# Kernel optimization log

Measured on AMD Instinct MI355X. Metric: run time of the kernel, lower is better.

Reference implementation:

```python
import jax, jax.numpy as jnp
import numpy as np

B, N, D, H = 8, 2048, 128, 8
HD = D // H  # head_depth = 16
CLIP = 10.0
INF = 1e10
THETA = 10000.0
SCALE_BASE = 512.0
LOGIT_SCALE = float(np.log(400.0) / np.log(50.0) / np.sqrt(HD))


def _rotate_half(x):
    # interleaved pairs: (x1, x2) -> (-x2, x1)
    x1 = x[..., ::2]
    x2 = x[..., 1::2]
    return jnp.stack((-x2, x1), axis=-1).reshape(x.shape)


def _rope_xpos(n, hd):
    # rotary_embedding_torch RotaryEmbedding(dim=hd, use_xpos=True)
    inv_freq = 1.0 / (THETA ** (jnp.arange(0, hd, 2, dtype=jnp.float32) / hd))  # (hd/2,)
    t = jnp.arange(n, dtype=jnp.float32)
    freqs = t[:, None] * inv_freq[None, :]          # (n, hd/2)
    freqs = jnp.repeat(freqs, 2, axis=-1)           # (n, hd) interleaved dup
    sc = (jnp.arange(0, hd, 2, dtype=jnp.float32) + 0.4 * hd) / (1.4 * hd)  # (hd/2,)
    power = (t - (n // 2)) / SCALE_BASE             # centered positions
    scale = sc[None, :] ** power[:, None]           # (n, hd/2)
    scale = jnp.repeat(scale, 2, axis=-1)           # (n, hd)
    return freqs, scale


def setup_inputs() -> dict:
    key = jax.random.key(0)
    ks = jax.random.split(key, 7)
    stdv_qkv = 1.0 / np.sqrt(HD)
    stdv_out = 1.0 / np.sqrt(D)
    q = jax.random.normal(ks[0], (B, N, D), dtype=jnp.float32)
    k = jax.random.normal(ks[1], (B, N, D), dtype=jnp.float32)
    v = jax.random.normal(ks[2], (B, N, D), dtype=jnp.float32)
    Wq = jax.random.uniform(ks[3], (D, D), minval=-stdv_qkv, maxval=stdv_qkv, dtype=jnp.float32)
    Wk = jax.random.uniform(ks[4], (D, D), minval=-stdv_qkv, maxval=stdv_qkv, dtype=jnp.float32)
    Wv = jax.random.uniform(ks[5], (D, D), minval=-stdv_qkv, maxval=stdv_qkv, dtype=jnp.float32)
    Wout = jax.random.uniform(ks[6], (D, D), minval=-stdv_out, maxval=stdv_out, dtype=jnp.float32)
    mask = jnp.zeros((B, N, 1), dtype=bool)
    return {"q": q, "k": k, "v": v, "Wq": Wq, "Wk": Wk, "Wv": Wv, "Wout": Wout, "mask": mask}


def reference(q, k, v, Wq, Wk, Wv, Wout, mask):
    def split_heads(t, W):
        # torch Linear (bias=False): t @ W.T, then (B,N,H,HD) -> (B,H,N,HD)
        return (t @ W.T).reshape(B, N, H, HD).transpose(0, 2, 1, 3)

    Qh = split_heads(q, Wq)
    Kh = split_heads(k, Wk)
    Vh = split_heads(v, Wv)

    freqs, scale = _rope_xpos(N, HD)  # (N, HD) each, broadcast over (B,H,N,HD)
    cos, sin = jnp.cos(freqs), jnp.sin(freqs)
    Qr = Qh * (cos * scale) + _rotate_half(Qh) * (sin * scale)
    inv_scale = 1.0 / scale
    Kr = Kh * (cos * inv_scale) + _rotate_half(Kh) * (sin * inv_scale)

    logits = jnp.einsum('bhqd,bhkd->bhqk', Qr, Kr) * LOGIT_SCALE
    logits = CLIP * jnp.tanh(logits)
    # mask: (B,N,1) bool, True -> masked; broadcast to (B,1,1,N)
    logits = jnp.where(mask[:, None, None, :, 0], -INF, logits)
    probs = jax.nn.softmax(logits, axis=-1)
    out = jnp.einsum('bhqk,bhkd->bhqd', probs, Vh)
    out = out.transpose(0, 2, 1, 3).reshape(B, N, D)
    return out @ Wout.T
```

## Files before the change

kernel.cpp:

```cpp
#include <hip/hip_runtime.h>
#include <math.h>

#define BB 8
#define NN 2048
#define DD 128
#define HH 8

typedef _Float16 v4h __attribute__((ext_vector_type(4)));
typedef _Float16 v8h __attribute__((ext_vector_type(8)));
typedef float    v4f __attribute__((ext_vector_type(4)));
typedef float    v16f __attribute__((ext_vector_type(16)));

__device__ __forceinline__ v4f zero4() { v4f z = {0.f, 0.f, 0.f, 0.f}; return z; }
__device__ __forceinline__ v16f zero16() {
    v16f z;
    #pragma unroll
    for (int i = 0; i < 16; ++i) z[i] = 0.f;
    return z;
}

__device__ __forceinline__ v4f mfma16(v4h a, v4h b, v4f c) {
    return __builtin_amdgcn_mfma_f32_16x16x16f16(a, b, c, 0, 0, 0);
}
__device__ __forceinline__ v16f mfma32(v8h a, v8h b, v16f c) {
    return __builtin_amdgcn_mfma_f32_32x32x16_f16(a, b, c, 0, 0, 0);
}

__device__ __forceinline__ float fexp2(float x) {
#if __has_builtin(__builtin_amdgcn_exp2f)
    return __builtin_amdgcn_exp2f(x);
#else
    return __expf(x * 0.69314718055994531f);
#endif
}

#define QSCALE 1.10478088f
#define C1F 14.426950408889634f
#define C2F 28.853900817779268f

__global__ __launch_bounds__(256) void prep_kernel(
    const float* __restrict__ Wq, const float* __restrict__ Wk,
    const float* __restrict__ Wv, const float* __restrict__ Wo,
    _Float16* __restrict__ WH, _Float16* __restrict__ WoH,
    float* __restrict__ rtab)
{
    int tid = blockIdx.x * 256 + threadIdx.x;
    int m = tid >> 14, i = tid & 16383;
    const float* src = (m == 0) ? Wq : (m == 1) ? Wk : (m == 2) ? Wv : Wo;
    float wv = src[i];
    if (m < 3) WH[m * 16384 + i] = (_Float16)wv;
    else       WoH[i] = (_Float16)wv;

    if (tid < NN * 16) {
        int t = tid >> 4, hd = tid & 15, j = hd >> 1;
        const float invf_tab[8] = {1.f, 0.31622776601683794f, 0.1f, 0.031622776601683791f,
                                   0.01f, 0.0031622776601683794f, 0.001f, 0.00031622776601683794f};
        float freq = (float)t * invf_tab[j];
        float c = cosf(freq), s = sinf(freq);
        float scf = ((float)(2 * j) + 6.4f) / 22.4f;
        float pw  = ((float)t - 1024.0f) / 512.0f;
        float scl = exp2f(pw * log2f(scf));
        rtab[0 * NN * 16 + tid] = c * scl * QSCALE;
        rtab[1 * NN * 16 + tid] = s * scl * QSCALE;
        float is = 1.0f / scl;
        rtab[2 * NN * 16 + tid] = c * is;
        rtab[3 * NN * 16 + tid] = s * is;
    }
}

__global__ __launch_bounds__(256) void proj_rope_kernel(
    const float* __restrict__ q, const float* __restrict__ k, const float* __restrict__ v,
    const _Float16* __restrict__ WH, const float* __restrict__ rtab,
    _Float16* __restrict__ Qr, _Float16* __restrict__ Kr, _Float16* __restrict__ VT)
{
    __shared__ __align__(16) _Float16 xb[64][136];
    const int tid = threadIdx.x;
    const int m  = blockIdx.y;
    const int r0 = blockIdx.x * 64;
    const int b  = r0 >> 11;
    const int n0 = r0 & 2047;

    const float* s = ((m == 0) ? q : (m == 1) ? k : v) + (size_t)r0 * 128;
    #pragma unroll
    for (int i = 0; i < 8; ++i) {
        int u = tid + i * 256;
        int row = u >> 5, c4 = (u & 31) * 4;
        v4f f = *(const v4f*)(s + row * 128 + c4);
        v4h hv; hv[0]=(_Float16)f[0]; hv[1]=(_Float16)f[1]; hv[2]=(_Float16)f[2]; hv[3]=(_Float16)f[3];
        *(v4h*)&xb[row][c4] = hv;
    }
    __syncthreads();

    const int w = tid >> 6, lane = tid & 63;
    const int l16 = lane & 15, quad = lane >> 4;

    v4h xf[8];
    #pragma unroll
    for (int kt = 0; kt < 8; ++kt)
        xf[kt] = *(const v4h*)&xb[w * 16 + l16][kt * 16 + quad * 4];
    const _Float16* Wm = WH + m * 16384;
    v4f acc[8];
    #pragma unroll
    for (int ct = 0; ct < 8; ++ct) acc[ct] = zero4();
    #pragma unroll
    for (int kt = 0; kt < 8; ++kt) {
        #pragma unroll
        for (int ct = 0; ct < 8; ++ct) {
            v4h wf = *(const v4h*)(Wm + (ct * 16 + l16) * 128 + kt * 16 + quad * 4);
            if (m < 2) acc[ct] = mfma16(wf, xf[kt], acc[ct]);
            else       acc[ct] = mfma16(xf[kt], wf, acc[ct]);
        }
    }
    if (m < 2) {
        const float* tc = rtab + (m == 0 ? 0 : 2 * NN * 16);
        const float* ts = tc + NN * 16;
        const int n = n0 + w * 16 + l16;
        _Float16* dst = (m == 0 ? Qr : Kr);
        #pragma unroll
        for (int ct = 0; ct < 8; ++ct) {
            v4f cs = *(const v4f*)(tc + n * 16 + quad * 4);
            v4f sn = *(const v4f*)(ts + n * 16 + quad * 4);
            v4f a = acc[ct];
            v4f rot; rot[0] = -a[1]; rot[1] = a[0]; rot[2] = -a[3]; rot[3] = a[2];
            v4h o;
            #pragma unroll
            for (int r = 0; r < 4; ++r) o[r] = (_Float16)(a[r] * cs[r] + rot[r] * sn[r]);
            *(v4h*)(dst + ((size_t)(b * 8 + ct) * NN + n) * 16 + quad * 4) = o;
        }
    } else {
        #pragma unroll
        for (int ct = 0; ct < 8; ++ct) {
            v4f a = acc[ct];
            v4h o;
            #pragma unroll
            for (int r = 0; r < 4; ++r) o[r] = (_Float16)a[r];
            *(v4h*)(VT + ((size_t)(b * 8 + ct) * 16 + l16) * NN + n0 + w * 16 + quad * 4) = o;
        }
    }
}

__global__ __launch_bounds__(256, 4) void attn_kernel(
    const _Float16* __restrict__ Qr, const _Float16* __restrict__ Kr,
    const _Float16* __restrict__ VT, const unsigned char* __restrict__ mask,
    _Float16* __restrict__ Obuf)
{
    __shared__ __align__(16) char smem[15360];
    _Float16* Kt = (_Float16*)smem;
    _Float16* Ve = (_Float16*)(smem + 6144);
    float*    av = (float*)(smem + 14848);

    const int tid = threadIdx.x;
    const int bh = blockIdx.x >> 4;
    const int qt = blockIdx.x & 15;
    const int b = bh >> 3, h = bh & 7;
    const int q0 = qt * 128;
    const int w = tid >> 6, lane = tid & 63;
    const int l32 = lane & 31, hi = lane >> 5;

    const int qrow = q0 + w * 32 + l32;
    v8h qf = *(const v8h*)(Qr + ((size_t)bh * NN + qrow) * 16 + hi * 8);

    {
        v8h one8;
        #pragma unroll
        for (int i = 0; i < 8; ++i) one8[i] = (_Float16)1.f;
        *(v8h*)(Ve + (16 + (tid >> 4)) * 136 + (tid & 15) * 8) = one8;
    }

    v16f acc = zero16();

    const int krow = tid >> 1, kpar = tid & 1;
    const int vhd = tid >> 4, vg = tid & 15;
    const _Float16* Kbase = Kr + (size_t)bh * NN * 16;
    const _Float16* Vbase = VT + ((size_t)bh * 16 + vhd) * NN;
    const unsigned char* mbase = mask + b * NN;

    v8h kv = *(const v8h*)(Kbase + (size_t)krow * 16 + kpar * 8);
    v8h vv = *(const v8h*)(Vbase + vg * 8);
    float adv = 0.f;
    if (tid < 128) adv = mbase[tid] ? -1e30f : C1F;

    for (int it = 0; it < 16; ++it) {
        __syncthreads();
        *(v8h*)(Kt + krow * 24 + kpar * 8) = kv;
        {
            _Float16* vb = Ve + vhd * 136 + (vg >> 1) * 16 + (vg & 1) * 4;
            v4h lo4, hi4;
            lo4[0]=vv[0]; lo4[1]=vv[1]; lo4[2]=vv[2]; lo4[3]=vv[3];
            hi4[0]=vv[4]; hi4[1]=vv[5]; hi4[2]=vv[6]; hi4[3]=vv[7];
            *(v4h*)(vb)     = lo4;
            *(v4h*)(vb + 8) = hi4;
        }
        if (tid < 128) av[tid] = adv;
        if (it < 15) {
            const int k0n = (it + 1) * 128;
            kv = *(const v8h*)(Kbase + (size_t)(k0n + krow) * 16 + kpar * 8);
            vv = *(const v8h*)(Vbase + k0n + vg * 8);
            if (tid < 128) adv = mbase[k0n + tid] ? -1e30f : C1F;
        }
        __syncthreads();

        #pragma unroll
        for (int kc = 0; kc < 4; ++kc) {
            v8h kf = *(const v8h*)(Kt + (kc * 32 + l32) * 24 + hi * 8);
            v16f sv = mfma32(kf, qf, zero16());

            v4f ad[4];
            #pragma unroll
            for (int gg = 0; gg < 4; ++gg)
                ad[gg] = *(const v4f*)(av + kc * 32 + gg * 8 + hi * 4);

            float p[16];
            #pragma unroll
            for (int r = 0; r < 16; ++r) {
                float u  = fexp2(sv[r]);
                float rc = __builtin_amdgcn_rcpf(u + 1.f);
                p[r] = fexp2(__builtin_fmaf(rc, -C2F, ad[r >> 2][r & 3]));
            }

            #pragma unroll
            for (int c2 = 0; c2 < 2; ++c2) {
                v8h pa;
                #pragma unroll
                for (int j = 0; j < 8; ++j) pa[j] = (_Float16)p[c2 * 8 + j];
                v8h vf = *(const v8h*)(Ve + l32 * 136 + (kc * 2 + c2) * 16 + hi * 8);
                acc = mfma32(pa, vf, acc);
            }
        }
    }

    float rs[16];
    #pragma unroll
    for (int r = 0; r < 16; ++r) rs[r] = __shfl_xor(acc[r], 16, 64);

    __syncthreads();
    _Float16* myOt = (_Float16*)smem + w * 768;
    if (!(lane & 16)) {
        int j = lane & 15;
        #pragma unroll
        for (int r = 0; r < 16; ++r) {
            int qr = (r & 3) + 8 * (r >> 2) + 4 * hi;
            myOt[qr * 24 + j] = (_Float16)(acc[r] * __builtin_amdgcn_rcpf(rs[r]));
        }
    }
    asm volatile("s_waitcnt lgkmcnt(0)" ::: "memory");
    v8h ov = *(const v8h*)(myOt + (lane >> 1) * 24 + (lane & 1) * 8);
    *(v8h*)(Obuf + ((size_t)(b * NN + q0 + w * 32 + (lane >> 1)) * 128) + h * 16 + (lane & 1) * 8) = ov;
}

__global__ __launch_bounds__(256) void outproj_kernel(
    const _Float16* __restrict__ Obuf, const _Float16* __restrict__ WoH,
    float* __restrict__ out)
{
    __shared__ __align__(16) _Float16 ob[64][136];
    const int tid = threadIdx.x;
    const int r0 = blockIdx.x * 64;
    const int ct0 = blockIdx.y * 2;
    #pragma unroll
    for (int i = 0; i < 8; ++i) {
        int u = tid + i * 256;
        int row = u >> 5, c4 = (u & 31) * 4;
        *(v4h*)&ob[row][c4] = *(const v4h*)(Obuf + (size_t)(r0 + row) * 128 + c4);
    }
    __syncthreads();
    const int w = tid >> 6, lane = tid & 63;
    const int l16 = lane & 15, quad = lane >> 4;
    v4h af[8];
    #pragma unroll
    for (int kt = 0; kt < 8; ++kt)
        af[kt] = *(const v4h*)&ob[w * 16 + l16][kt * 16 + quad * 4];
    v4f acc[2];
    #pragma unroll
    for (int c = 0; c < 2; ++c) acc[c] = zero4();
    #pragma unroll
    for (int kt = 0; kt < 8; ++kt)
        #pragma unroll
        for (int c = 0; c < 2; ++c) {
            v4h wf = *(const v4h*)(WoH + ((ct0 + c) * 16 + l16) * 128 + kt * 16 + quad * 4);
            acc[c] = mfma16(af[kt], wf, acc[c]);
        }
    #pragma unroll
    for (int c = 0; c < 2; ++c)
        #pragma unroll
        for (int r = 0; r < 4; ++r)
            out[(size_t)(r0 + w * 16 + quad * 4 + r) * 128 + (ct0 + c) * 16 + l16] = acc[c][r];
}

extern "C" void kernel_launch(void* const* d_in, const int* in_sizes, int n_in,
                              void* d_out, int out_size, void* d_ws, size_t ws_size,
                              hipStream_t stream)
{
    const float* q  = (const float*)d_in[0];
    const float* k  = (const float*)d_in[1];
    const float* v  = (const float*)d_in[2];
    const float* Wq = (const float*)d_in[3];
    const float* Wk = (const float*)d_in[4];
    const float* Wv = (const float*)d_in[5];
    const float* Wo = (const float*)d_in[6];
    const unsigned char* mask = (const unsigned char*)d_in[7];
    float* out = (float*)d_out;

    char* ws = (char*)d_ws;
    _Float16* WH   = (_Float16*)(ws);
    _Float16* WoH  = (_Float16*)(ws + 98304);
    float*    rtab = (float*)(ws + 131072);
    _Float16* Qr   = (_Float16*)(ws + 655360);
    _Float16* Kr   = (_Float16*)(ws + 4849664);
    _Float16* VTd  = (_Float16*)(ws + 9043968);
    _Float16* Obuf = (_Float16*)(ws + 13238272);

    prep_kernel<<<256, 256, 0, stream>>>(Wq, Wk, Wv, Wo, WH, WoH, rtab);
    proj_rope_kernel<<<dim3(256, 3), 256, 0, stream>>>(q, k, v, WH, rtab, Qr, Kr, VTd);
    attn_kernel<<<1024, 256, 0, stream>>>(Qr, Kr, VTd, mask, Obuf);
    outproj_kernel<<<dim3(256, 4), 256, 0, stream>>>(Obuf, WoH, out);
}
```

Baseline: 195.3 us.

## Drop prep kernel, fuse weight cast and RoPE table, double-buffer attention LDS

Removes the separate prep kernel. Weight fp32-to-fp16 conversion moves inline into the projection and output-projection loads, and the RoPE cos/sin/xpos table is computed per block into shared memory. The attention kernel double-buffers its K/V/mask LDS tiles so one of the two per-iteration barriers can be dropped. The costs are a kernel launch and the global rtab traffic traded for redundant trig and conversion work and doubled LDS use in attention, which may lower occupancy.

```diff
diff --git a/kernel.cpp b/kernel.cpp
--- a/kernel.cpp
+++ b/kernel.cpp
@@ -38,42 +38,14 @@
 #define C1F 14.426950408889634f
 #define C2F 28.853900817779268f
 
-__global__ __launch_bounds__(256) void prep_kernel(
-    const float* __restrict__ Wq, const float* __restrict__ Wk,
-    const float* __restrict__ Wv, const float* __restrict__ Wo,
-    _Float16* __restrict__ WH, _Float16* __restrict__ WoH,
-    float* __restrict__ rtab)
-{
-    int tid = blockIdx.x * 256 + threadIdx.x;
-    int m = tid >> 14, i = tid & 16383;
-    const float* src = (m == 0) ? Wq : (m == 1) ? Wk : (m == 2) ? Wv : Wo;
-    float wv = src[i];
-    if (m < 3) WH[m * 16384 + i] = (_Float16)wv;
-    else       WoH[i] = (_Float16)wv;
-
-    if (tid < NN * 16) {
-        int t = tid >> 4, hd = tid & 15, j = hd >> 1;
-        const float invf_tab[8] = {1.f, 0.31622776601683794f, 0.1f, 0.031622776601683791f,
-                                   0.01f, 0.0031622776601683794f, 0.001f, 0.00031622776601683794f};
-        float freq = (float)t * invf_tab[j];
-        float c = cosf(freq), s = sinf(freq);
-        float scf = ((float)(2 * j) + 6.4f) / 22.4f;
-        float pw  = ((float)t - 1024.0f) / 512.0f;
-        float scl = exp2f(pw * log2f(scf));
-        rtab[0 * NN * 16 + tid] = c * scl * QSCALE;
-        rtab[1 * NN * 16 + tid] = s * scl * QSCALE;
-        float is = 1.0f / scl;
-        rtab[2 * NN * 16 + tid] = c * is;
-        rtab[3 * NN * 16 + tid] = s * is;
-    }
-}
-
 __global__ __launch_bounds__(256) void proj_rope_kernel(
     const float* __restrict__ q, const float* __restrict__ k, const float* __restrict__ v,
-    const _Float16* __restrict__ WH, const float* __restrict__ rtab,
+    const float* __restrict__ Wq, const float* __restrict__ Wk, const float* __restrict__ Wv,
     _Float16* __restrict__ Qr, _Float16* __restrict__ Kr, _Float16* __restrict__ VT)
 {
     __shared__ __align__(16) _Float16 xb[64][136];
+    __shared__ __align__(16) float ctc[64][16];
+    __shared__ __align__(16) float cts[64][16];
     const int tid = threadIdx.x;
     const int m  = blockIdx.y;
     const int r0 = blockIdx.x * 64;
@@ -89,6 +61,30 @@
         v4h hv; hv[0]=(_Float16)f[0]; hv[1]=(_Float16)f[1]; hv[2]=(_Float16)f[2]; hv[3]=(_Float16)f[3];
         *(v4h*)&xb[row][c4] = hv;
     }
+
+    if (m < 2) {
+        #pragma unroll
+        for (int i = 0; i < 2; ++i) {
+            int u2 = tid + i * 256;
+            int tl = u2 >> 3, j = u2 & 7;
+            float fa = (j & 4) ? 1e-2f : 1.f;
+            float fb = (j & 2) ? 1e-1f : 1.f;
+            float fc = (j & 1) ? 0.31622776601683794f : 1.f;
+            float invf = fa * fb * fc;
+            float t = (float)(n0 + tl);
+            float freq = t * invf;
+            float c = cosf(freq), si = sinf(freq);
+            float scf = ((float)(2 * j) + 6.4f) / 22.4f;
+            float pw  = (t - 1024.0f) / 512.0f;
+            float scl = exp2f(pw * log2f(scf));
+            float sc  = (m == 0) ? scl * QSCALE : 1.0f / scl;
+            float cc = c * sc, ss = si * sc;
+            ctc[tl][2 * j]     = cc;
+            ctc[tl][2 * j + 1] = cc;
+            cts[tl][2 * j]     = ss;
+            cts[tl][2 * j + 1] = ss;
+        }
+    }
     __syncthreads();
 
     const int w = tid >> 6, lane = tid & 63;
@@ -98,7 +94,7 @@
     #pragma unroll
     for (int kt = 0; kt < 8; ++kt)
         xf[kt] = *(const v4h*)&xb[w * 16 + l16][kt * 16 + quad * 4];
-    const _Float16* Wm = WH + m * 16384;
+    const float* Wm = (m == 0) ? Wq : (m == 1) ? Wk : Wv;
     v4f acc[8];
     #pragma unroll
     for (int ct = 0; ct < 8; ++ct) acc[ct] = zero4();
@@ -106,20 +102,20 @@
     for (int kt = 0; kt < 8; ++kt) {
         #pragma unroll
         for (int ct = 0; ct < 8; ++ct) {
-            v4h wf = *(const v4h*)(Wm + (ct * 16 + l16) * 128 + kt * 16 + quad * 4);
+            v4f wv = *(const v4f*)(Wm + (ct * 16 + l16) * 128 + kt * 16 + quad * 4);
+            v4h wf; wf[0]=(_Float16)wv[0]; wf[1]=(_Float16)wv[1]; wf[2]=(_Float16)wv[2]; wf[3]=(_Float16)wv[3];
             if (m < 2) acc[ct] = mfma16(wf, xf[kt], acc[ct]);
             else       acc[ct] = mfma16(xf[kt], wf, acc[ct]);
         }
     }
     if (m < 2) {
-        const float* tc = rtab + (m == 0 ? 0 : 2 * NN * 16);
-        const float* ts = tc + NN * 16;
-        const int n = n0 + w * 16 + l16;
+        const int tl = w * 16 + l16;
+        const int n = n0 + tl;
         _Float16* dst = (m == 0 ? Qr : Kr);
         #pragma unroll
         for (int ct = 0; ct < 8; ++ct) {
-            v4f cs = *(const v4f*)(tc + n * 16 + quad * 4);
-            v4f sn = *(const v4f*)(ts + n * 16 + quad * 4);
+            v4f cs = *(const v4f*)&ctc[tl][quad * 4];
+            v4f sn = *(const v4f*)&cts[tl][quad * 4];
             v4f a = acc[ct];
             v4f rot; rot[0] = -a[1]; rot[1] = a[0]; rot[2] = -a[3]; rot[3] = a[2];
             v4h o;
@@ -144,10 +140,7 @@
     const _Float16* __restrict__ VT, const unsigned char* __restrict__ mask,
     _Float16* __restrict__ Obuf)
 {
-    __shared__ __align__(16) char smem[15360];
-    _Float16* Kt = (_Float16*)smem;
-    _Float16* Ve = (_Float16*)(smem + 6144);
-    float*    av = (float*)(smem + 14848);
+    __shared__ __align__(16) char smem[30720];
 
     const int tid = threadIdx.x;
     const int bh = blockIdx.x >> 4;
@@ -164,7 +157,9 @@
         v8h one8;
         #pragma unroll
         for (int i = 0; i < 8; ++i) one8[i] = (_Float16)1.f;
-        *(v8h*)(Ve + (16 + (tid >> 4)) * 136 + (tid & 15) * 8) = one8;
+        int rr = 16 + (tid >> 4), cc = (tid & 15) * 8;
+        *(v8h*)((_Float16*)(smem +         6144) + rr * 136 + cc) = one8;
+        *(v8h*)((_Float16*)(smem + 15360 + 6144) + rr * 136 + cc) = one8;
     }
 
     v16f acc = zero16();
@@ -181,7 +176,11 @@
     if (tid < 128) adv = mbase[tid] ? -1e30f : C1F;
 
     for (int it = 0; it < 16; ++it) {
-        __syncthreads();
+        char* buf = smem + (it & 1) * 15360;
+        _Float16* Kt = (_Float16*)buf;
+        _Float16* Ve = (_Float16*)(buf + 6144);
+        float*    av = (float*)(buf + 14848);
+
         *(v8h*)(Kt + krow * 24 + kpar * 8) = kv;
         {
             _Float16* vb = Ve + vhd * 136 + (vg >> 1) * 16 + (vg & 1) * 4;
@@ -233,7 +232,6 @@
     #pragma unroll
     for (int r = 0; r < 16; ++r) rs[r] = __shfl_xor(acc[r], 16, 64);
 
-    __syncthreads();
     _Float16* myOt = (_Float16*)smem + w * 768;
     if (!(lane & 16)) {
         int j = lane & 15;
@@ -249,7 +247,7 @@
 }
 
 __global__ __launch_bounds__(256) void outproj_kernel(
-    const _Float16* __restrict__ Obuf, const _Float16* __restrict__ WoH,
+    const _Float16* __restrict__ Obuf, const float* __restrict__ Wo,
     float* __restrict__ out)
 {
     __shared__ __align__(16) _Float16 ob[64][136];
@@ -276,7 +274,8 @@
     for (int kt = 0; kt < 8; ++kt)
         #pragma unroll
         for (int c = 0; c < 2; ++c) {
-            v4h wf = *(const v4h*)(WoH + ((ct0 + c) * 16 + l16) * 128 + kt * 16 + quad * 4);
+            v4f wv = *(const v4f*)(Wo + ((ct0 + c) * 16 + l16) * 128 + kt * 16 + quad * 4);
+            v4h wf; wf[0]=(_Float16)wv[0]; wf[1]=(_Float16)wv[1]; wf[2]=(_Float16)wv[2]; wf[3]=(_Float16)wv[3];
             acc[c] = mfma16(af[kt], wf, acc[c]);
         }
     #pragma unroll
@@ -301,16 +300,12 @@
     float* out = (float*)d_out;
 
     char* ws = (char*)d_ws;
-    _Float16* WH   = (_Float16*)(ws);
-    _Float16* WoH  = (_Float16*)(ws + 98304);
-    float*    rtab = (float*)(ws + 131072);
-    _Float16* Qr   = (_Float16*)(ws + 655360);
-    _Float16* Kr   = (_Float16*)(ws + 4849664);
-    _Float16* VTd  = (_Float16*)(ws + 9043968);
-    _Float16* Obuf = (_Float16*)(ws + 13238272);
-
-    prep_kernel<<<256, 256, 0, stream>>>(Wq, Wk, Wv, Wo, WH, WoH, rtab);
-    proj_rope_kernel<<<dim3(256, 3), 256, 0, stream>>>(q, k, v, WH, rtab, Qr, Kr, VTd);
+    _Float16* Qr   = (_Float16*)(ws);
+    _Float16* Kr   = (_Float16*)(ws + 4194304);
+    _Float16* VTd  = (_Float16*)(ws + 8388608);
+    _Float16* Obuf = (_Float16*)(ws + 12582912);
+
+    proj_rope_kernel<<<dim3(256, 3), 256, 0, stream>>>(q, k, v, Wq, Wk, Wv, Qr, Kr, VTd);
     attn_kernel<<<1024, 256, 0, stream>>>(Qr, Kr, VTd, mask, Obuf);
-    outproj_kernel<<<dim3(256, 4), 256, 0, stream>>>(Obuf, WoH, out);
-}
+    outproj_kernel<<<dim3(256, 4), 256, 0, stream>>>(Obuf, Wo, out);
+}
```

Result: no change. 195.1 us (-0.1%).
